# Kernel tuning notes

Hardware: AMD Instinct MI355X
Metric: run time of the kernel (lower is better)

The kernel has to match this reference:

```python
import jax, jax.numpy as jnp
import numpy as np

B, T, C = 8, 2048, 1024
DFF = 4 * C
EPS = 1e-5


def _ln(h, w, b):
    mu = jnp.mean(h, axis=-1, keepdims=True)
    var = jnp.mean((h - mu) ** 2, axis=-1, keepdims=True)
    return (h - mu) * jax.lax.rsqrt(var + EPS) * w + b


def setup_inputs() -> dict:
    key = jax.random.key(0)
    ks = jax.random.split(key, 8)
    s = lambda fan_in: 1.0 / np.sqrt(fan_in)
    return {
        "x": jax.random.normal(ks[0], (B, T, C), jnp.float32),
        "w_router": jax.random.normal(ks[1], (1, C), jnp.float32) * s(C),
        "ln1_w": jnp.ones((C,), jnp.float32),
        "ln1_b": jnp.zeros((C,), jnp.float32),
        "w_qkv": jax.random.normal(ks[2], (3 * C, C), jnp.float32) * s(C),
        "b_qkv": jnp.zeros((3 * C,), jnp.float32),
        "w_o": jax.random.normal(ks[3], (C, C), jnp.float32) * s(C),
        "b_o": jnp.zeros((C,), jnp.float32),
        "ln2_w": jnp.ones((C,), jnp.float32),
        "ln2_b": jnp.zeros((C,), jnp.float32),
        "w_fc": jax.random.normal(ks[4], (DFF, C), jnp.float32) * s(C),
        "b_fc": jnp.zeros((DFF,), jnp.float32),
        "w_proj": jax.random.normal(ks[5], (C, DFF), jnp.float32) * s(DFF),
        "b_proj": jnp.zeros((C,), jnp.float32),
        "top_k": 1024,
        "n_head": 16,
    }


def _gpt2_block(h, ln1_w, ln1_b, w_qkv, b_qkv, w_o, b_o, ln2_w, ln2_b,
                w_fc, b_fc, w_proj, b_proj, n_head):
    Bq, S, Cm = h.shape
    dh = Cm // n_head
    a = _ln(h, ln1_w, ln1_b)
    qkv = a @ w_qkv.T + b_qkv                         # [B,S,3C]
    q, k, v = jnp.split(qkv, 3, axis=-1)
    q = q.reshape(Bq, S, n_head, dh)
    k = k.reshape(Bq, S, n_head, dh)
    v = v.reshape(Bq, S, n_head, dh)
    scores = jnp.einsum("bqhd,bkhd->bhqk", q, k) / np.sqrt(dh)
    causal = jnp.tril(jnp.ones((S, S), bool))
    scores = jnp.where(causal, scores, jnp.finfo(scores.dtype).min)
    probs = jax.nn.softmax(scores, axis=-1)
    attn = jnp.einsum("bhqk,bkhd->bqhd", probs, v).reshape(Bq, S, Cm)
    h = h + attn @ w_o.T + b_o
    m = _ln(h, ln2_w, ln2_b)
    mlp = jax.nn.gelu(m @ w_fc.T + b_fc, approximate=False) @ w_proj.T + b_proj
    return h + mlp


def reference(x, w_router, ln1_w, ln1_b, w_qkv, b_qkv, w_o, b_o,
              ln2_w, ln2_b, w_fc, b_fc, w_proj, b_proj, top_k, n_head):
    # STEP 1: router logits + top-k tokens (sorted by position)
    logits = (x @ w_router.T)[..., 0]                  # [B,T]
    weights, idx = jax.lax.top_k(logits, top_k)        # [B,K]
    order = jnp.argsort(idx, axis=1)
    idx = jnp.take_along_axis(idx, order, axis=1)
    weights = jnp.take_along_axis(weights, order, axis=1)
    # STEP 2: gather reduced sequence and run the block
    tokens = jnp.take_along_axis(x, idx[..., None], axis=1)   # [B,K,C]
    processed = _gpt2_block(tokens, ln1_w, ln1_b, w_qkv, b_qkv, w_o, b_o,
                            ln2_w, ln2_b, w_fc, b_fc, w_proj, b_proj, n_head)
    # STEP 3: weighted scatter-add combine
    src = processed * weights[..., None]
    out = jax.vmap(lambda xb, ib, sb: xb.at[ib].add(sb))(x, idx, src)
    return out
```

## Files before the change

kernel.cpp:

```cpp
#include <hip/hip_runtime.h>
#include <hip/hip_bf16.h>

#define B_ 8
#define T_ 2048
#define C_ 1024
#define S_ 1024
#define H_ 16
#define DH_ 64
#define DFF_ 4096
#define M_ (B_*S_)

typedef __attribute__((ext_vector_type(8))) short bf16x8;
typedef __attribute__((ext_vector_type(4))) float f32x4;

__device__ __forceinline__ short f2bf(float f) {
  __hip_bfloat16 h = __float2bfloat16(f);
  return *reinterpret_cast<short*>(&h);
}
__device__ __forceinline__ float bf2f(short s) {
  __hip_bfloat16 h = *reinterpret_cast<__hip_bfloat16*>(&s);
  return __bfloat162float(h);
}

typedef const __attribute__((address_space(1))) unsigned int* gas_p;
typedef __attribute__((address_space(3))) unsigned int* las_p;
__device__ __forceinline__ void gload_lds16(const void* g, void* l) {
  __builtin_amdgcn_global_load_lds((gas_p)g, (las_p)l, 16, 0, 0);
}

__global__ __launch_bounds__(256) void k_router(const float* __restrict__ x,
    const float* __restrict__ wr, float* __restrict__ logits) {
  int tok = blockIdx.x * 4 + (threadIdx.x >> 6);
  int l = threadIdx.x & 63;
  const float* xr = x + (size_t)tok * C_;
  float s = 0.f;
  #pragma unroll
  for (int j = 0; j < C_/64; ++j) s += xr[l + 64*j] * wr[l + 64*j];
  #pragma unroll
  for (int m = 32; m; m >>= 1) s += __shfl_xor(s, m);
  if (l == 0) logits[tok] = s;
}

__global__ __launch_bounds__(1024) void k_topk(const float* __restrict__ logits,
    int* __restrict__ idx, float* __restrict__ wts) {
  __shared__ unsigned long long key[2048];
  int b = blockIdx.x, t = threadIdx.x;
  for (int i = t; i < T_; i += 1024) {
    float v = logits[(size_t)b*T_ + i];
    unsigned u = __float_as_uint(v);
    unsigned so = u ^ ((u >> 31) ? 0xFFFFFFFFu : 0x80000000u);
    key[i] = ((unsigned long long)(~so) << 32) | (unsigned)i;
  }
  __syncthreads();
  for (int k = 2; k <= 2048; k <<= 1) {
    for (int j = k >> 1; j > 0; j >>= 1) {
      int i = ((t & ~(j-1)) << 1) | (t & (j-1));
      int ix = i | j;
      unsigned long long a = key[i], c = key[ix];
      bool up = ((i & k) == 0);
      if ((a > c) == up) { key[i] = c; key[ix] = a; }
      __syncthreads();
    }
  }
  unsigned long long a = key[t];
  __syncthreads();
  unsigned i0 = (unsigned)(a & 0xFFFFFFFFu);
  unsigned so = ~(unsigned)(a >> 32);
  unsigned bits = (so & 0x80000000u) ? (so ^ 0x80000000u) : ~so;
  key[t] = ((unsigned long long)i0 << 32) | bits;
  __syncthreads();
  for (int k = 2; k <= 1024; k <<= 1) {
    for (int j = k >> 1; j > 0; j >>= 1) {
      if (t < 512) {
        int i = ((t & ~(j-1)) << 1) | (t & (j-1));
        int ix = i | j;
        unsigned long long a2 = key[i], c2 = key[ix];
        bool up = ((i & k) == 0);
        if ((a2 > c2) == up) { key[i] = c2; key[ix] = a2; }
      }
      __syncthreads();
    }
  }
  idx[(size_t)b*S_ + t] = (int)(key[t] >> 32);
  wts[(size_t)b*S_ + t] = __uint_as_float((unsigned)(key[t] & 0xFFFFFFFFu));
}

__global__ __launch_bounds__(256) void k_cvt(const float* __restrict__ s,
    short* __restrict__ d, int n4) {
  int i = blockIdx.x * 256 + threadIdx.x;
  if (i >= n4) return;
  float4 v = ((const float4*)s)[i];
  short4 o;
  o.x = f2bf(v.x); o.y = f2bf(v.y); o.z = f2bf(v.z); o.w = f2bf(v.w);
  ((short4*)d)[i] = o;
}

template<bool GATHER>
__global__ __launch_bounds__(256) void k_ln(const float* __restrict__ x,
    const int* __restrict__ idx, float* __restrict__ hbuf,
    short* __restrict__ obf, const float* __restrict__ g,
    const float* __restrict__ beta) {
  __shared__ float red[8];
  int row = blockIdx.x;
  const float* src;
  if (GATHER) {
    int b = row >> 10, k = row & 1023;
    src = x + ((size_t)b*T_ + idx[b*S_ + k]) * C_;
  } else {
    src = hbuf + (size_t)row * C_;
  }
  int t = threadIdx.x;
  float4 v = *(const float4*)(src + t*4);
  float s  = v.x + v.y + v.z + v.w;
  float s2 = v.x*v.x + v.y*v.y + v.z*v.z + v.w*v.w;
  #pragma unroll
  for (int m = 32; m; m >>= 1) { s += __shfl_xor(s, m); s2 += __shfl_xor(s2, m); }
  int w = t >> 6, lane = t & 63;
  if (lane == 0) { red[w] = s; red[w+4] = s2; }
  __syncthreads();
  s  = red[0]+red[1]+red[2]+red[3];
  s2 = red[4]+red[5]+red[6]+red[7];
  float mu = s * (1.f/(float)C_);
  float var = s2 * (1.f/(float)C_) - mu*mu;
  float rs = rsqrtf(var + 1e-5f);
  int c0 = t*4;
  float4 gw = *(const float4*)(g + c0);
  float4 bw = *(const float4*)(beta + c0);
  short4 o;
  o.x = f2bf((v.x-mu)*rs*gw.x + bw.x);
  o.y = f2bf((v.y-mu)*rs*gw.y + bw.y);
  o.z = f2bf((v.z-mu)*rs*gw.z + bw.z);
  o.w = f2bf((v.w-mu)*rs*gw.w + bw.w);
  *(short4*)(obf + (size_t)row*C_ + c0) = o;
  if (GATHER) *(float4*)(hbuf + (size_t)row*C_ + c0) = v;
}

#define EPI_BF16 0
#define EPI_GELU 1
#define EPI_ADD32 2

__device__ __forceinline__ float gelu_fast(float v) {
  float z = 0.7978845608f * (v + 0.044715f * v * v * v);
  float e = __expf(2.f * z);
  return v - v * __builtin_amdgcn_rcpf(e + 1.f);
}

template<int BM, int BN, int EPI>
__global__ __launch_bounds__(256) void k_gemm4(
    const short* __restrict__ A, int lda,
    const short* __restrict__ Bp, int ldb,
    void* __restrict__ Cp, int ldc,
    const float* __restrict__ bias,
    int nNt, int Ktot) {
  constexpr int ACH = BM*64/8/256;
  constexpr int BCH = BN*64/8/256;
  __shared__ short As[BM*64];
  __shared__ short Bs[BN*64];
  int nwg = gridDim.x, orig = blockIdx.x;
  int q8 = nwg >> 3, r8 = nwg & 7;
  int xcd = orig & 7, loc = orig >> 3;
  int wg = (xcd < r8 ? xcd*(q8+1) : r8*(q8+1) + (xcd-r8)*q8) + loc;
  int bm = wg / nNt, bn = wg % nNt;
  const short* Ar = A + (size_t)bm*BM*lda;
  const short* Br = Bp + (size_t)bn*BN*ldb;
  constexpr int WM = BM/2, WN = BN/2, FM = WM/16, FN = WN/16;
  int t = threadIdx.x, lane = t & 63, w = t >> 6;
  int wm = w >> 1, wn = w & 1;
  int lr = lane & 15, kq = lane >> 4;
  f32x4 acc[FM][FN] = {};
  for (int k0 = 0; k0 < Ktot; k0 += 64) {
    #pragma unroll
    for (int c = 0; c < ACH; ++c) {
      int ch = c*256 + t;
      int row = ch >> 3, sq = (ch & 7) ^ (row & 7);
      gload_lds16(Ar + (size_t)row*lda + (k0 + sq*8), &As[ch*8]);
    }
    #pragma unroll
    for (int c = 0; c < BCH; ++c) {
      int ch = c*256 + t;
      int row = ch >> 3, sq = (ch & 7) ^ (row & 7);
      gload_lds16(Br + (size_t)row*ldb + (k0 + sq*8), &Bs[ch*8]);
    }
    asm volatile("s_waitcnt vmcnt(0)" ::: "memory");
    __syncthreads();
    bf16x8 af[2][FM], bfv[2][FN];
    #pragma unroll
    for (int ks = 0; ks < 2; ++ks) {
      #pragma unroll
      for (int i = 0; i < FM; ++i) {
        int ra = wm*WM + i*16 + lr;
        af[ks][i] = *(const bf16x8*)&As[ra*64 + ((((ks<<2)+kq) ^ (ra & 7)) << 3)];
      }
      #pragma unroll
      for (int j = 0; j < FN; ++j) {
        int rb = wn*WN + j*16 + lr;
        bfv[ks][j] = *(const bf16x8*)&Bs[rb*64 + ((((ks<<2)+kq) ^ (rb & 7)) << 3)];
      }
    }
    #pragma unroll
    for (int ks = 0; ks < 2; ++ks)
      #pragma unroll
      for (int i = 0; i < FM; ++i)
        #pragma unroll
        for (int j = 0; j < FN; ++j)
          acc[i][j] = __builtin_amdgcn_mfma_f32_16x16x32_bf16(bfv[ks][j], af[ks][i], acc[i][j], 0, 0, 0);
    __syncthreads();
  }
  int mrow0 = bm*BM + wm*WM + lr;
  int ncol0 = bn*BN + wn*WN + (kq << 2);
  #pragma unroll
  for (int i = 0; i < FM; ++i) {
    int row = mrow0 + i*16;
    #pragma unroll
    for (int j = 0; j < FN; ++j) {
      int col = ncol0 + j*16;
      float4 bv = bias ? *(const float4*)(bias + col) : make_float4(0.f,0.f,0.f,0.f);
      float v0 = acc[i][j][0] + bv.x, v1 = acc[i][j][1] + bv.y;
      float v2 = acc[i][j][2] + bv.z, v3 = acc[i][j][3] + bv.w;
      if (EPI == EPI_ADD32) {
        float* Co = (float*)Cp + (size_t)row*ldc + col;
        float4 old = *(float4*)Co;
        old.x += v0; old.y += v1; old.z += v2; old.w += v3;
        *(float4*)Co = old;
      } else {
        if (EPI == EPI_GELU) {
          v0 = gelu_fast(v0); v1 = gelu_fast(v1);
          v2 = gelu_fast(v2); v3 = gelu_fast(v3);
        }
        short4 o; o.x = f2bf(v0); o.y = f2bf(v1); o.z = f2bf(v2); o.w = f2bf(v3);
        *(short4*)((short*)Cp + (size_t)row*ldc + col) = o;
      }
    }
  }
}

__global__ __launch_bounds__(256) void k_vt(const short* __restrict__ qkv,
                                            short* __restrict__ vt) {
  __shared__ short tile[64][65];
  int blk = blockIdx.x;
  int s0 = (blk & 15) << 6;
  int bh = blk >> 4;
  int b = bh >> 4, h = bh & 15;
  const short* src = qkv + (size_t)b*S_*3*C_ + 2*C_ + h*DH_;
  int t = threadIdx.x;
  #pragma unroll
  for (int it = 0; it < 16; ++it) {
    int e = it*256 + t;
    int r = e >> 6, d = e & 63;
    tile[d][r] = src[(size_t)(s0 + r)*3*C_ + d];
  }
  __syncthreads();
  short* dst = vt + (size_t)bh*DH_*S_ + s0;
  #pragma unroll
  for (int it = 0; it < 16; ++it) {
    int e = it*256 + t;
    int d2 = e >> 6, c = e & 63;
    dst[(size_t)d2*S_ + c] = tile[d2][c];
  }
}

__global__ __launch_bounds__(256, 4) void k_fattn(
    const short* __restrict__ qkv, const short* __restrict__ vt,
    short* __restrict__ attnb) {
  __shared__ short Ks[2][64*64];
  __shared__ short Ps[4][32*72];
  int qt = blockIdx.x;
  int bh = blockIdx.y;
  int b = bh >> 4, h = bh & 15;
  int t = threadIdx.x, lane = t & 63, w = t >> 6;
  int lr = lane & 15, kq = lane >> 4;
  const short* Qbase = qkv + ((size_t)b*S_ + qt*128)*3*C_ + h*DH_;
  const short* Kbase = qkv + (size_t)b*S_*3*C_ + C_ + h*DH_;
  const short* Vtb   = vt + (size_t)bh*DH_*S_;

  short* Qs = &Ks[0][0];
  #pragma unroll
  for (int c = 0; c < 4; ++c) {
    int ch = c*256 + t;
    int row = ch >> 3, sq = (ch & 7) ^ (row & 7);
    gload_lds16(Qbase + (size_t)row*3*C_ + sq*8, &Qs[ch*8]);
  }
  asm volatile("s_waitcnt vmcnt(0)" ::: "memory");
  __builtin_amdgcn_s_barrier();
  bf16x8 qf[2][2];
  #pragma unroll
  for (int ks = 0; ks < 2; ++ks)
    #pragma unroll
    for (int i = 0; i < 2; ++i) {
      int rq = w*32 + i*16 + lr;
      qf[ks][i] = *(const bf16x8*)&Qs[rq*64 + ((((ks<<2)+kq) ^ (rq & 7)) << 3)];
    }
  asm volatile("s_waitcnt lgkmcnt(0)" ::: "memory");
  __builtin_amdgcn_sched_barrier(0);
  __builtin_amdgcn_s_barrier();

  auto stageK = [&](int buf, int jj) {
    #pragma unroll
    for (int c = 0; c < 2; ++c) {
      int ch = c*256 + t;
      int row = ch >> 3, sq = (ch & 7) ^ (row & 7);
      gload_lds16(Kbase + (size_t)(jj*64 + row)*3*C_ + sq*8, &Ks[buf][ch*8]);
    }
  };
  stageK(0, 0);

  f32x4 o[2][4] = {};
  float m_i[2] = {-3.0e38f, -3.0e38f};
  float l_i[2] = {0.f, 0.f};
  short* Pw = &Ps[w][0];
  int NTl = 2*qt + 2;

  for (int jj = 0; jj < NTl; ++jj) {
    int cur = jj & 1;
    asm volatile("s_waitcnt vmcnt(0)" ::: "memory");
    __builtin_amdgcn_s_barrier();
    if (jj + 1 < NTl) stageK(cur ^ 1, jj + 1);

    f32x4 s[2][4] = {};
    #pragma unroll
    for (int ks = 0; ks < 2; ++ks) {
      bf16x8 kf[4];
      #pragma unroll
      for (int j = 0; j < 4; ++j) {
        int rk = j*16 + lr;
        kf[j] = *(const bf16x8*)&Ks[cur][rk*64 + ((((ks<<2)+kq) ^ (rk & 7)) << 3)];
      }
      #pragma unroll
      for (int i = 0; i < 2; ++i)
        #pragma unroll
        for (int j = 0; j < 4; ++j)
          s[i][j] = __builtin_amdgcn_mfma_f32_16x16x32_bf16(kf[j], qf[ks][i], s[i][j], 0, 0, 0);
    }

    bool maskTile = (jj >= 2*qt);
    #pragma unroll
    for (int i = 0; i < 2; ++i) {
      int qrow = qt*128 + w*32 + i*16 + lr;
      float rmax = -3.0e38f;
      #pragma unroll
      for (int j = 0; j < 4; ++j)
        #pragma unroll
        for (int r = 0; r < 4; ++r) {
          int colg = jj*64 + j*16 + (kq<<2) + r;
          float v = s[i][j][r] * 0.125f;
          if (maskTile && colg > qrow) v = -3.0e38f;
          s[i][j][r] = v;
          rmax = fmaxf(rmax, v);
        }
      rmax = fmaxf(rmax, __shfl_xor(rmax, 16));
      rmax = fmaxf(rmax, __shfl_xor(rmax, 32));
      float mnew = fmaxf(m_i[i], rmax);
      float alpha = __expf(m_i[i] - mnew);
      m_i[i] = mnew;
      float rsum = 0.f;
      #pragma unroll
      for (int j = 0; j < 4; ++j)
        #pragma unroll
        for (int r = 0; r < 4; ++r) {
          float pv = __expf(s[i][j][r] - mnew);
          s[i][j][r] = pv;
          rsum += pv;
        }
      rsum += __shfl_xor(rsum, 16);
      rsum += __shfl_xor(rsum, 32);
      l_i[i] = l_i[i]*alpha + rsum;
      #pragma unroll
      for (int jo = 0; jo < 4; ++jo)
        #pragma unroll
        for (int r = 0; r < 4; ++r)
          o[i][jo][r] *= alpha;
    }

    #pragma unroll
    for (int i = 0; i < 2; ++i)
      #pragma unroll
      for (int j = 0; j < 4; ++j) {
        short4 pk;
        pk.x = f2bf(s[i][j][0]); pk.y = f2bf(s[i][j][1]);
        pk.z = f2bf(s[i][j][2]); pk.w = f2bf(s[i][j][3]);
        *(short4*)&Pw[(i*16 + lr)*72 + j*16 + (kq<<2)] = pk;
      }
    asm volatile("s_waitcnt lgkmcnt(0)" ::: "memory");
    __builtin_amdgcn_sched_barrier(0);

    #pragma unroll
    for (int sstep = 0; sstep < 2; ++sstep) {
      bf16x8 pf[2], vf[4];
      #pragma unroll
      for (int i = 0; i < 2; ++i)
        pf[i] = *(const bf16x8*)&Pw[(i*16 + lr)*72 + sstep*32 + (kq<<3)];
      #pragma unroll
      for (int jo = 0; jo < 4; ++jo)
        vf[jo] = *(const bf16x8*)&Vtb[(size_t)(jo*16 + lr)*S_ + jj*64 + sstep*32 + (kq<<3)];
      #pragma unroll
      for (int i = 0; i < 2; ++i)
        #pragma unroll
        for (int jo = 0; jo < 4; ++jo)
          o[i][jo] = __builtin_amdgcn_mfma_f32_16x16x32_bf16(vf[jo], pf[i], o[i][jo], 0, 0, 0);
    }
  }

  #pragma unroll
  for (int i = 0; i < 2; ++i) {
    float inv = 1.f / l_i[i];
    int q = qt*128 + w*32 + i*16 + lr;
    #pragma unroll
    for (int jo = 0; jo < 4; ++jo) {
      int d = jo*16 + (kq<<2);
      short4 ov;
      ov.x = f2bf(o[i][jo][0]*inv); ov.y = f2bf(o[i][jo][1]*inv);
      ov.z = f2bf(o[i][jo][2]*inv); ov.w = f2bf(o[i][jo][3]*inv);
      *(short4*)&attnb[((size_t)b*S_ + q)*C_ + h*DH_ + d] = ov;
    }
  }
}

__global__ void k_copy(const float* __restrict__ src, float* __restrict__ dst,
                       size_t n4) {
  size_t i = (size_t)blockIdx.x*256 + threadIdx.x;
  size_t stride = (size_t)gridDim.x*256;
  for (; i < n4; i += stride) ((float4*)dst)[i] = ((const float4*)src)[i];
}

__global__ __launch_bounds__(256) void k_scatter(const float* __restrict__ x,
    const int* __restrict__ idx, const float* __restrict__ wts,
    const float* __restrict__ hbuf, float* __restrict__ out) {
  int row = blockIdx.x;
  int b = row >> 10, k = row & 1023;
  int tk = idx[(size_t)b*S_ + k];
  float wv = wts[(size_t)b*S_ + k];
  size_t o  = ((size_t)b*T_ + tk)*C_ + threadIdx.x*4;
  size_t hs = (size_t)row*C_ + threadIdx.x*4;
  float4 xv = *(const float4*)(x + o);
  float4 hv = *(const float4*)(hbuf + hs);
  xv.x += wv*hv.x; xv.y += wv*hv.y; xv.z += wv*hv.z; xv.w += wv*hv.w;
  *(float4*)(out + o) = xv;
}

extern "C" void kernel_launch(void* const* d_in, const int* in_sizes, int n_in,
                              void* d_out, int out_size, void* d_ws, size_t ws_size,
                              hipStream_t stream) {
  const float* x     = (const float*)d_in[0];
  const float* wrt   = (const float*)d_in[1];
  const float* ln1w  = (const float*)d_in[2];
  const float* ln1b  = (const float*)d_in[3];
  const float* wqkv  = (const float*)d_in[4];
  const float* bqkv  = (const float*)d_in[5];
  const float* wo    = (const float*)d_in[6];
  const float* bo    = (const float*)d_in[7];
  const float* ln2w  = (const float*)d_in[8];
  const float* ln2b  = (const float*)d_in[9];
  const float* wfc   = (const float*)d_in[10];
  const float* bfc   = (const float*)d_in[11];
  const float* wproj = (const float*)d_in[12];
  const float* bproj = (const float*)d_in[13];
  float* out = (float*)d_out;

  char* p = (char*)d_ws;
  auto alloc = [&](size_t bytes) {
    char* r = p; p += (bytes + 255) & ~(size_t)255; return r;
  };
  float* logits = (float*)alloc((size_t)B_*T_*4);
  int*   idx    = (int*)  alloc((size_t)B_*S_*4);
  float* wts    = (float*)alloc((size_t)B_*S_*4);
  float* hbuf   = (float*)alloc((size_t)M_*C_*4);
  short* abuf   = (short*)alloc((size_t)M_*C_*2);
  short* qkvb   = (short*)alloc((size_t)M_*3*C_*2);
  short* vtb    = (short*)alloc((size_t)B_*H_*DH_*S_*2);
  short* attnb  = (short*)alloc((size_t)M_*C_*2);
  short* fcb    = (short*)alloc((size_t)M_*DFF_*2);
  short* wqkvb  = (short*)alloc((size_t)3*C_*C_*2);
  short* wob    = (short*)alloc((size_t)C_*C_*2);
  short* wfcb   = (short*)alloc((size_t)DFF_*C_*2);
  short* wprojb = (short*)alloc((size_t)C_*DFF_*2);
  if (ws_size < (size_t)(p - (char*)d_ws)) return;

  k_cvt<<<dim3(3*C_*C_/4/256), dim3(256), 0, stream>>>(wqkv, wqkvb, 3*C_*C_/4);
  k_cvt<<<dim3(C_*C_/4/256),   dim3(256), 0, stream>>>(wo, wob, C_*C_/4);
  k_cvt<<<dim3(DFF_*C_/4/256), dim3(256), 0, stream>>>(wfc, wfcb, DFF_*C_/4);
  k_cvt<<<dim3(C_*DFF_/4/256), dim3(256), 0, stream>>>(wproj, wprojb, C_*DFF_/4);

  k_router<<<dim3(B_*T_/4), dim3(256), 0, stream>>>(x, wrt, logits);
  k_topk<<<dim3(B_), dim3(1024), 0, stream>>>(logits, idx, wts);

  k_ln<true><<<dim3(M_), dim3(256), 0, stream>>>(x, idx, hbuf, abuf, ln1w, ln1b);

  k_gemm4<128,128,EPI_BF16>
    <<<dim3((M_/128)*(3*C_/128)), dim3(256), 0, stream>>>(
      abuf, C_, wqkvb, C_, qkvb, 3*C_, bqkv, 3*C_/128, C_);

  k_vt<<<dim3(B_*H_*(S_/64)), dim3(256), 0, stream>>>(qkvb, vtb);

  k_fattn<<<dim3(S_/128, B_*H_), dim3(256), 0, stream>>>(qkvb, vtb, attnb);

  k_gemm4<128,128,EPI_ADD32>
    <<<dim3((M_/128)*(C_/128)), dim3(256), 0, stream>>>(
      attnb, C_, wob, C_, hbuf, C_, bo, C_/128, C_);

  k_ln<false><<<dim3(M_), dim3(256), 0, stream>>>(nullptr, nullptr, hbuf, abuf, ln2w, ln2b);

  k_gemm4<128,128,EPI_GELU>
    <<<dim3((M_/128)*(DFF_/128)), dim3(256), 0, stream>>>(
      abuf, C_, wfcb, C_, fcb, DFF_, bfc, DFF_/128, C_);

  k_gemm4<128,128,EPI_ADD32>
    <<<dim3((M_/128)*(C_/128)), dim3(256), 0, stream>>>(
      fcb, DFF_, wprojb, DFF_, hbuf, C_, bproj, C_/128, DFF_);

  k_copy<<<dim3(2048), dim3(256), 0, stream>>>(x, out, (size_t)B_*T_*C_/4);
  k_scatter<<<dim3(M_), dim3(256), 0, stream>>>(x, idx, wts, hbuf, out);
}
```

Before: 533.5 us.

## Triple-buffer GEMM LDS tiles with async prefetch and 256x128 tiles

Replaces the single-buffered 128x128 GEMM with a 256x128, 512-thread kernel that keeps three LDS stages and prefetches two k-tiles ahead. Partial vmcnt waits and one barrier per iteration replace the full drain and double sync, so global loads can overlap MFMA work. It uses 144KB of LDS per block, which may limit occupancy despite the launch bound of 2, and it assumes the M and N dimensions divide the new tile sizes.

New measurement: 547.9 us. +2.7%, slower.

```diff
diff --git a/kernel.cpp b/kernel.cpp
--- a/kernel.cpp
+++ b/kernel.cpp
@@ -145,17 +145,16 @@
   return v - v * __builtin_amdgcn_rcpf(e + 1.f);
 }
 
-template<int BM, int BN, int EPI>
-__global__ __launch_bounds__(256) void k_gemm4(
+template<int EPI>
+__global__ __launch_bounds__(512, 2) void k_gemm5(
     const short* __restrict__ A, int lda,
     const short* __restrict__ Bp, int ldb,
     void* __restrict__ Cp, int ldc,
     const float* __restrict__ bias,
     int nNt, int Ktot) {
-  constexpr int ACH = BM*64/8/256;
-  constexpr int BCH = BN*64/8/256;
-  __shared__ short As[BM*64];
-  __shared__ short Bs[BN*64];
+  constexpr int BM = 256, BN = 128;
+  __shared__ short As[3][BM*64];
+  __shared__ short Bs[3][BN*64];
   int nwg = gridDim.x, orig = blockIdx.x;
   int q8 = nwg >> 3, r8 = nwg & 7;
   int xcd = orig & 7, loc = orig >> 3;
@@ -163,56 +162,68 @@
   int bm = wg / nNt, bn = wg % nNt;
   const short* Ar = A + (size_t)bm*BM*lda;
   const short* Br = Bp + (size_t)bn*BN*ldb;
-  constexpr int WM = BM/2, WN = BN/2, FM = WM/16, FN = WN/16;
   int t = threadIdx.x, lane = t & 63, w = t >> 6;
   int wm = w >> 1, wn = w & 1;
   int lr = lane & 15, kq = lane >> 4;
-  f32x4 acc[FM][FN] = {};
-  for (int k0 = 0; k0 < Ktot; k0 += 64) {
-    #pragma unroll
-    for (int c = 0; c < ACH; ++c) {
-      int ch = c*256 + t;
+
+  auto stage = [&](int buf, int kt) {
+    int k0 = kt << 6;
+    #pragma unroll
+    for (int c = 0; c < 4; ++c) {
+      int ch = c*512 + t;
       int row = ch >> 3, sq = (ch & 7) ^ (row & 7);
-      gload_lds16(Ar + (size_t)row*lda + (k0 + sq*8), &As[ch*8]);
-    }
-    #pragma unroll
-    for (int c = 0; c < BCH; ++c) {
-      int ch = c*256 + t;
+      gload_lds16(Ar + (size_t)row*lda + (k0 + sq*8), &As[buf][ch*8]);
+    }
+    #pragma unroll
+    for (int c = 0; c < 2; ++c) {
+      int ch = c*512 + t;
       int row = ch >> 3, sq = (ch & 7) ^ (row & 7);
-      gload_lds16(Br + (size_t)row*ldb + (k0 + sq*8), &Bs[ch*8]);
-    }
-    asm volatile("s_waitcnt vmcnt(0)" ::: "memory");
-    __syncthreads();
-    bf16x8 af[2][FM], bfv[2][FN];
+      gload_lds16(Br + (size_t)row*ldb + (k0 + sq*8), &Bs[buf][ch*8]);
+    }
+  };
+
+  f32x4 acc[4][4] = {};
+  int NT = Ktot >> 6;
+  stage(0, 0);
+  if (NT > 1) stage(1, 1);
+  for (int kt = 0; kt < NT; ++kt) {
+    int cur = kt % 3;
+    if (kt + 1 < NT) asm volatile("s_waitcnt vmcnt(6)" ::: "memory");
+    else             asm volatile("s_waitcnt vmcnt(0)" ::: "memory");
+    __builtin_amdgcn_s_barrier();
+    __builtin_amdgcn_sched_barrier(0);
+    if (kt + 2 < NT) stage((kt + 2) % 3, kt + 2);
+    bf16x8 af[2][4], bfv[2][4];
     #pragma unroll
     for (int ks = 0; ks < 2; ++ks) {
       #pragma unroll
-      for (int i = 0; i < FM; ++i) {
-        int ra = wm*WM + i*16 + lr;
-        af[ks][i] = *(const bf16x8*)&As[ra*64 + ((((ks<<2)+kq) ^ (ra & 7)) << 3)];
+      for (int i = 0; i < 4; ++i) {
+        int ra = wm*64 + i*16 + lr;
+        af[ks][i] = *(const bf16x8*)&As[cur][ra*64 + ((((ks<<2)+kq) ^ (ra & 7)) << 3)];
       }
       #pragma unroll
-      for (int j = 0; j < FN; ++j) {
-        int rb = wn*WN + j*16 + lr;
-        bfv[ks][j] = *(const bf16x8*)&Bs[rb*64 + ((((ks<<2)+kq) ^ (rb & 7)) << 3)];
+      for (int j = 0; j < 4; ++j) {
+        int rb = wn*64 + j*16 + lr;
+        bfv[ks][j] = *(const bf16x8*)&Bs[cur][rb*64 + ((((ks<<2)+kq) ^ (rb & 7)) << 3)];
       }
     }
+    asm volatile("s_waitcnt lgkmcnt(0)" ::: "memory");
+    __builtin_amdgcn_sched_barrier(0);
     #pragma unroll
     for (int ks = 0; ks < 2; ++ks)
       #pragma unroll
-      for (int i = 0; i < FM; ++i)
+      for (int i = 0; i < 4; ++i)
         #pragma unroll
-        for (int j = 0; j < FN; ++j)
+        for (int j = 0; j < 4; ++j)
           acc[i][j] = __builtin_amdgcn_mfma_f32_16x16x32_bf16(bfv[ks][j], af[ks][i], acc[i][j], 0, 0, 0);
-    __syncthreads();
-  }
-  int mrow0 = bm*BM + wm*WM + lr;
-  int ncol0 = bn*BN + wn*WN + (kq << 2);
-  #pragma unroll
-  for (int i = 0; i < FM; ++i) {
+  }
+  int mrow0 = bm*BM + wm*64 + lr;
+  int ncol0 = bn*BN + wn*64 + (kq << 2);
+  #pragma unroll
+  for (int i = 0; i < 4; ++i) {
     int row = mrow0 + i*16;
     #pragma unroll
-    for (int j = 0; j < FN; ++j) {
+    for (int j = 0; j < 4; ++j) {
       int col = ncol0 + j*16;
       float4 bv = bias ? *(const float4*)(bias + col) : make_float4(0.f,0.f,0.f,0.f);
       float v0 = acc[i][j][0] + bv.x, v1 = acc[i][j][1] + bv.y;
@@ -485,26 +496,22 @@
 
   k_ln<true><<<dim3(M_), dim3(256), 0, stream>>>(x, idx, hbuf, abuf, ln1w, ln1b);
 
-  k_gemm4<128,128,EPI_BF16>
-    <<<dim3((M_/128)*(3*C_/128)), dim3(256), 0, stream>>>(
+  k_gemm5<EPI_BF16><<<dim3((M_/256)*(3*C_/128)), dim3(512), 0, stream>>>(
       abuf, C_, wqkvb, C_, qkvb, 3*C_, bqkv, 3*C_/128, C_);
 
   k_vt<<<dim3(B_*H_*(S_/64)), dim3(256), 0, stream>>>(qkvb, vtb);
 
   k_fattn<<<dim3(S_/128, B_*H_), dim3(256), 0, stream>>>(qkvb, vtb, attnb);
 
-  k_gemm4<128,128,EPI_ADD32>
-    <<<dim3((M_/128)*(C_/128)), dim3(256), 0, stream>>>(
+  k_gemm5<EPI_ADD32><<<dim3((M_/256)*(C_/128)), dim3(512), 0, stream>>>(
       attnb, C_, wob, C_, hbuf, C_, bo, C_/128, C_);
 
   k_ln<false><<<dim3(M_), dim3(256), 0, stream>>>(nullptr, nullptr, hbuf, abuf, ln2w, ln2b);
 
-  k_gemm4<128,128,EPI_GELU>
-    <<<dim3((M_/128)*(DFF_/128)), dim3(256), 0, stream>>>(
+  k_gemm5<EPI_GELU><<<dim3((M_/256)*(DFF_/128)), dim3(512), 0, stream>>>(
       abuf, C_, wfcb, C_, fcb, DFF_, bfc, DFF_/128, C_);
 
-  k_gemm4<128,128,EPI_ADD32>
-    <<<dim3((M_/128)*(C_/128)), dim3(256), 0, stream>>>(
+  k_gemm5<EPI_ADD32><<<dim3((M_/256)*(C_/128)), dim3(512), 0, stream>>>(
       fcb, DFF_, wprojb, DFF_, hbuf, C_, bproj, C_/128, DFF_);
 
   k_copy<<<dim3(2048), dim3(256), 0, stream>>>(x, out, (size_t)B_*T_*C_/4);
```

## Double-buffer GEMM LDS tiles and fuse copy with scatter via inverse token map

Applied to the files above, without the earlier changes.

The GEMM kernel now uses two LDS buffers, so the global-to-LDS load of the next K tile is issued before the MFMAs on the current tile. It also drops one barrier per iteration and requests two workgroups per CU through launch bounds. The separate full-tensor copy and scatter kernels are replaced by one combine pass per output row. That pass uses a token-to-slot map written by top-k, which removes an extra read/write sweep of the output. The double-buffered loop no longer has an explicit vmcnt wait before the barrier, so correctness depends on the async LDS loads having completed in time; LDS use also doubles, which may limit occupancy.

Measured after the change: 493.8 us. -7.4%, faster.

```diff
diff --git a/kernel.cpp b/kernel.cpp
--- a/kernel.cpp
+++ b/kernel.cpp
@@ -41,8 +41,13 @@
   if (l == 0) logits[tok] = s;
 }
 
+__global__ __launch_bounds__(256) void k_initmap(int* __restrict__ map) {
+  int i = blockIdx.x*256 + threadIdx.x;
+  ((int4*)map)[i] = make_int4(-1, -1, -1, -1);
+}
+
 __global__ __launch_bounds__(1024) void k_topk(const float* __restrict__ logits,
-    int* __restrict__ idx, float* __restrict__ wts) {
+    int* __restrict__ idx, float* __restrict__ wts, int* __restrict__ map) {
   __shared__ unsigned long long key[2048];
   int b = blockIdx.x, t = threadIdx.x;
   for (int i = t; i < T_; i += 1024) {
@@ -81,8 +86,10 @@
       __syncthreads();
     }
   }
-  idx[(size_t)b*S_ + t] = (int)(key[t] >> 32);
+  int tok = (int)(key[t] >> 32);
+  idx[(size_t)b*S_ + t] = tok;
   wts[(size_t)b*S_ + t] = __uint_as_float((unsigned)(key[t] & 0xFFFFFFFFu));
+  map[(size_t)b*T_ + tok] = t;
 }
 
 __global__ __launch_bounds__(256) void k_cvt(const float* __restrict__ s,
@@ -146,7 +153,7 @@
 }
 
 template<int BM, int BN, int EPI>
-__global__ __launch_bounds__(256) void k_gemm4(
+__global__ __launch_bounds__(256, 2) void k_gemm7(
     const short* __restrict__ A, int lda,
     const short* __restrict__ Bp, int ldb,
     void* __restrict__ Cp, int ldc,
@@ -154,8 +161,8 @@
     int nNt, int Ktot) {
   constexpr int ACH = BM*64/8/256;
   constexpr int BCH = BN*64/8/256;
-  __shared__ short As[BM*64];
-  __shared__ short Bs[BN*64];
+  __shared__ short As[2][BM*64];
+  __shared__ short Bs[2][BN*64];
   int nwg = gridDim.x, orig = blockIdx.x;
   int q8 = nwg >> 3, r8 = nwg & 7;
   int xcd = orig & 7, loc = orig >> 3;
@@ -167,34 +174,43 @@
   int t = threadIdx.x, lane = t & 63, w = t >> 6;
   int wm = w >> 1, wn = w & 1;
   int lr = lane & 15, kq = lane >> 4;
-  f32x4 acc[FM][FN] = {};
-  for (int k0 = 0; k0 < Ktot; k0 += 64) {
+
+  auto stage = [&](int buf, int k0) {
     #pragma unroll
     for (int c = 0; c < ACH; ++c) {
       int ch = c*256 + t;
       int row = ch >> 3, sq = (ch & 7) ^ (row & 7);
-      gload_lds16(Ar + (size_t)row*lda + (k0 + sq*8), &As[ch*8]);
+      gload_lds16(Ar + (size_t)row*lda + (k0 + sq*8), &As[buf][ch*8]);
     }
     #pragma unroll
     for (int c = 0; c < BCH; ++c) {
       int ch = c*256 + t;
       int row = ch >> 3, sq = (ch & 7) ^ (row & 7);
-      gload_lds16(Br + (size_t)row*ldb + (k0 + sq*8), &Bs[ch*8]);
-    }
-    asm volatile("s_waitcnt vmcnt(0)" ::: "memory");
-    __syncthreads();
+      gload_lds16(Br + (size_t)row*ldb + (k0 + sq*8), &Bs[buf][ch*8]);
+    }
+  };
+
+  f32x4 acc[FM][FN] = {};
+  int NT = Ktot >> 6;
+  stage(0, 0);
+  __syncthreads();
+  for (int kt = 0; kt < NT; ++kt) {
+    int cur = kt & 1;
+    if (kt + 1 < NT) stage(cur ^ 1, (kt + 1) << 6);
+    const short* Ab = As[cur];
+    const short* Bb = Bs[cur];
     bf16x8 af[2][FM], bfv[2][FN];
     #pragma unroll
     for (int ks = 0; ks < 2; ++ks) {
       #pragma unroll
       for (int i = 0; i < FM; ++i) {
         int ra = wm*WM + i*16 + lr;
-        af[ks][i] = *(const bf16x8*)&As[ra*64 + ((((ks<<2)+kq) ^ (ra & 7)) << 3)];
+        af[ks][i] = *(const bf16x8*)&Ab[ra*64 + ((((ks<<2)+kq) ^ (ra & 7)) << 3)];
       }
       #pragma unroll
       for (int j = 0; j < FN; ++j) {
         int rb = wn*WN + j*16 + lr;
-        bfv[ks][j] = *(const bf16x8*)&Bs[rb*64 + ((((ks<<2)+kq) ^ (rb & 7)) << 3)];
+        bfv[ks][j] = *(const bf16x8*)&Bb[rb*64 + ((((ks<<2)+kq) ^ (rb & 7)) << 3)];
       }
     }
     #pragma unroll
@@ -204,7 +220,7 @@
         #pragma unroll
         for (int j = 0; j < FN; ++j)
           acc[i][j] = __builtin_amdgcn_mfma_f32_16x16x32_bf16(bfv[ks][j], af[ks][i], acc[i][j], 0, 0, 0);
-    __syncthreads();
+    if (kt + 1 < NT) __syncthreads();
   }
   int mrow0 = bm*BM + wm*WM + lr;
   int ncol0 = bn*BN + wn*WN + (kq << 2);
@@ -415,25 +431,20 @@
   }
 }
 
-__global__ void k_copy(const float* __restrict__ src, float* __restrict__ dst,
-                       size_t n4) {
-  size_t i = (size_t)blockIdx.x*256 + threadIdx.x;
-  size_t stride = (size_t)gridDim.x*256;
-  for (; i < n4; i += stride) ((float4*)dst)[i] = ((const float4*)src)[i];
-}
-
-__global__ __launch_bounds__(256) void k_scatter(const float* __restrict__ x,
-    const int* __restrict__ idx, const float* __restrict__ wts,
+__global__ __launch_bounds__(256) void k_combine(const float* __restrict__ x,
+    const int* __restrict__ map, const float* __restrict__ wts,
     const float* __restrict__ hbuf, float* __restrict__ out) {
   int row = blockIdx.x;
-  int b = row >> 10, k = row & 1023;
-  int tk = idx[(size_t)b*S_ + k];
-  float wv = wts[(size_t)b*S_ + k];
-  size_t o  = ((size_t)b*T_ + tk)*C_ + threadIdx.x*4;
-  size_t hs = (size_t)row*C_ + threadIdx.x*4;
+  int b = row >> 11;
+  int m = map[row];
+  size_t o = (size_t)row*C_ + threadIdx.x*4;
   float4 xv = *(const float4*)(x + o);
-  float4 hv = *(const float4*)(hbuf + hs);
-  xv.x += wv*hv.x; xv.y += wv*hv.y; xv.z += wv*hv.z; xv.w += wv*hv.w;
+  if (m >= 0) {
+    float wv = wts[(size_t)b*S_ + m];
+    const float* hr = hbuf + ((size_t)b*S_ + m)*C_ + threadIdx.x*4;
+    float4 hv = *(const float4*)hr;
+    xv.x += wv*hv.x; xv.y += wv*hv.y; xv.z += wv*hv.z; xv.w += wv*hv.w;
+  }
   *(float4*)(out + o) = xv;
 }
 
@@ -463,6 +474,7 @@
   float* logits = (float*)alloc((size_t)B_*T_*4);
   int*   idx    = (int*)  alloc((size_t)B_*S_*4);
   float* wts    = (float*)alloc((size_t)B_*S_*4);
+  int*   map    = (int*)  alloc((size_t)B_*T_*4);
   float* hbuf   = (float*)alloc((size_t)M_*C_*4);
   short* abuf   = (short*)alloc((size_t)M_*C_*2);
   short* qkvb   = (short*)alloc((size_t)M_*3*C_*2);
@@ -481,32 +493,28 @@
   k_cvt<<<dim3(C_*DFF_/4/256), dim3(256), 0, stream>>>(wproj, wprojb, C_*DFF_/4);
 
   k_router<<<dim3(B_*T_/4), dim3(256), 0, stream>>>(x, wrt, logits);
-  k_topk<<<dim3(B_), dim3(1024), 0, stream>>>(logits, idx, wts);
+  k_initmap<<<dim3(B_*T_/4/256), dim3(256), 0, stream>>>(map);
+  k_topk<<<dim3(B_), dim3(1024), 0, stream>>>(logits, idx, wts, map);
 
   k_ln<true><<<dim3(M_), dim3(256), 0, stream>>>(x, idx, hbuf, abuf, ln1w, ln1b);
 
-  k_gemm4<128,128,EPI_BF16>
-    <<<dim3((M_/128)*(3*C_/128)), dim3(256), 0, stream>>>(
+  k_gemm7<128,128,EPI_BF16><<<dim3((M_/128)*(3*C_/128)), dim3(256), 0, stream>>>(
       abuf, C_, wqkvb, C_, qkvb, 3*C_, bqkv, 3*C_/128, C_);
 
   k_vt<<<dim3(B_*H_*(S_/64)), dim3(256), 0, stream>>>(qkvb, vtb);
 
   k_fattn<<<dim3(S_/128, B_*H_), dim3(256), 0, stream>>>(qkvb, vtb, attnb);
 
-  k_gemm4<128,128,EPI_ADD32>
-    <<<dim3((M_/128)*(C_/128)), dim3(256), 0, stream>>>(
+  k_gemm7<128,128,EPI_ADD32><<<dim3((M_/128)*(C_/128)), dim3(256), 0, stream>>>(
       attnb, C_, wob, C_, hbuf, C_, bo, C_/128, C_);
 
   k_ln<false><<<dim3(M_), dim3(256), 0, stream>>>(nullptr, nullptr, hbuf, abuf, ln2w, ln2b);
 
-  k_gemm4<128,128,EPI_GELU>
-    <<<dim3((M_/128)*(DFF_/128)), dim3(256), 0, stream>>>(
+  k_gemm7<128,128,EPI_GELU><<<dim3((M_/128)*(DFF_/128)), dim3(256), 0, stream>>>(
       abuf, C_, wfcb, C_, fcb, DFF_, bfc, DFF_/128, C_);
 
-  k_gemm4<128,128,EPI_ADD32>
-    <<<dim3((M_/128)*(C_/128)), dim3(256), 0, stream>>>(
+  k_gemm7<128,128,EPI_ADD32><<<dim3((M_/128)*(C_/128)), dim3(256), 0, stream>>>(
       fcb, DFF_, wprojb, DFF_, hbuf, C_, bproj, C_/128, DFF_);
 
-  k_copy<<<dim3(2048), dim3(256), 0, stream>>>(x, out, (size_t)B_*T_*C_/4);
-  k_scatter<<<dim3(M_), dim3(256), 0, stream>>>(x, idx, wts, hbuf, out);
-}
+  k_combine<<<dim3(B_*T_), dim3(256), 0, stream>>>(x, map, wts, hbuf, out);
+}
```
